# Optimization experiments

Measured on AMD Instinct MI355X. Metric: run time of the kernel, lower is better.

Reference implementation:

```python
import jax, jax.numpy as jnp
import numpy as np

GRID = 3
K = GRID ** 3          # keypoints per proposal (grid rep)
RADIUS = 0.2
NSAMPLE = 16


def _rotz(t):
    c, s = jnp.cos(t), jnp.sin(t)
    z, o = jnp.zeros_like(t), jnp.ones_like(t)
    return jnp.stack([jnp.stack([c, -s, z], -1),
                      jnp.stack([s,  c, z], -1),
                      jnp.stack([z,  z, o], -1)], -2)  # [..., 3, 3]


def _grid_keypoints(boxes, origins, heading):
    # boxes: [B,P,6] = (left,back,down,right,front,up) absolute distances from origin
    B, P, _ = boxes.shape
    ii = jnp.stack(jnp.meshgrid(jnp.arange(GRID), jnp.arange(GRID), jnp.arange(GRID), indexing='ij'), -1)
    dense = ii.reshape(K, 3).astype(boxes.dtype)  # same order as ones(g,g,g).nonzero()
    size = boxes[..., 0:3] + boxes[..., 3:6]                       # [B,P,3]
    local = (dense + 0.5) / GRID * size[:, :, None, :] - boxes[..., None, 0:3]  # [B,P,K,3]
    R = _rotz(heading)                                             # [B,P,3,3]
    pts = jnp.einsum('bpkc,bpcd->bpkd', local, R) + origins[:, :, None, :]
    return pts.reshape(B, P * K, 3)


def _ball_query(key_pts, seed_xyz):
    # key_pts [B,M,3], seed_xyz [B,N,3] -> neighbor indices [B,M,NSAMPLE]
    N = seed_xyz.shape[1]
    d2 = (jnp.sum(key_pts ** 2, -1)[:, :, None]
          + jnp.sum(seed_xyz ** 2, -1)[:, None, :]
          - 2.0 * jnp.einsum('bmc,bnc->bmn', key_pts, seed_xyz))   # [B,M,N]
    cand = jnp.where(d2 < RADIUS ** 2, jnp.arange(N, dtype=jnp.int32), N)
    idx = -jax.lax.top_k(-cand, NSAMPLE)[0]  # first NSAMPLE in-radius indices, ascending
    first = idx[..., 0:1]
    fill = jnp.where(first == N, 0, first)   # empty ball -> index 0 (CUDA kernel default)
    return jnp.where(idx == N, fill, idx)


def _forward(seed_xyz, seed_features, boxes, origins, heading, W1, b1, W2, b2, W3, b3, Wr, br):
    B, P = boxes.shape[:2]
    key_pts = _grid_keypoints(boxes, origins, heading)             # [B,M,3], M=P*K
    idx = _ball_query(key_pts, seed_xyz)                           # [B,M,S]
    b_idx = jnp.arange(B)[:, None, None]
    gx = seed_xyz[b_idx, idx]                                      # [B,M,S,3]
    gf = jnp.transpose(seed_features, (0, 2, 1))[b_idx, idx]       # [B,M,S,C]
    gxyz = (gx - key_pts[:, :, None, :]) / RADIUS                  # normalize_xyz=True
    x = jnp.concatenate([gxyz, gf], -1)                            # use_xyz: [B,M,S,3+C]
    x = jax.nn.relu(x @ W1 + b1)                                   # shared per-point MLP
    x = jax.nn.relu(x @ W2 + b2)
    x = jax.nn.relu(x @ W3 + b3)
    x = jnp.max(x, axis=2)                                         # max-pool over ball -> [B,M,32]
    f = x.reshape(B, P, K, 32)
    # original: [B,32,M] -> view(B,32,P,K) -> transpose(2,3) -> reshape(B,32*K,P)
    f = jnp.transpose(f, (0, 1, 3, 2)).reshape(B, P, 32 * K)       # channel-major (c*K+k) layout
    out = f @ Wr.T + br                                            # 1x1 conv reduce -> [B,P,128]
    return jnp.transpose(out, (0, 2, 1))                           # [B,128,P]


def setup_inputs() -> dict:
    key = jax.random.key(0)
    ks = jax.random.split(key, 9)
    B, N, C, P = 2, 1024, 256, 256
    return {
        'seed_xyz': jax.random.normal(ks[0], (B, N, 3), jnp.float32),
        'seed_features': jax.random.normal(ks[1], (B, C, N), jnp.float32),
        'boxes': jax.random.uniform(ks[2], (B, P, 6), jnp.float32, 0.1, 1.0),
        'origins': jax.random.normal(ks[3], (B, P, 3), jnp.float32),
        'heading': jax.random.uniform(ks[4], (B, P), jnp.float32, 0.0, 6.2831853),
        'W1': jax.random.normal(ks[5], (C + 3, 128), jnp.float32) * 0.05,
        'b1': jnp.zeros((128,), jnp.float32),
        'W2': jax.random.normal(ks[6], (128, 64), jnp.float32) * 0.05,
        'b2': jnp.zeros((64,), jnp.float32),
        'W3': jax.random.normal(ks[7], (64, 32), jnp.float32) * 0.05,
        'b3': jnp.zeros((32,), jnp.float32),
        'Wr': jax.random.normal(ks[8], (128, 32 * K), jnp.float32) * 0.05,
        'br': jnp.zeros((128,), jnp.float32),
    }


def reference(seed_xyz, seed_features, boxes, origins, heading, W1, b1, W2, b2, W3, b3, Wr, br):
    return _forward(seed_xyz, seed_features, boxes, origins, heading, W1, b1, W2, b2, W3, b3, Wr, br)
```

## Files before the change

### kernel.cpp

```cpp
#include <hip/hip_runtime.h>

#define B_ 2
#define N_ 1024
#define C_ 256
#define P_ 256
#define K_ 27
#define M_ (P_ * K_)
#define TOTKP (B_ * M_)
#define NS 16
#define R2C 0.04f
#define QDIM 864


__global__ __launch_bounds__(128) void fpre_k(
    const float* __restrict__ sf, const float* __restrict__ W1,
    const float* __restrict__ b1, float* __restrict__ F)
{
    __shared__ __align__(16) float ssf[C_ * 8];
    int tid = threadIdx.x;
    int bid = blockIdx.x;
    int b = bid >> 7;
    int n0 = (bid & 127) * 8;
    for (int e = tid; e < C_ * 8; e += 128) {
        int c = e >> 3, i = e & 7;
        ssf[e] = sf[(b * C_ + c) * N_ + n0 + i];
    }
    __syncthreads();
    int j = tid;
    float acc[8];
    float bj = b1[j];
#pragma unroll
    for (int i = 0; i < 8; i++) acc[i] = bj;
#pragma unroll 4
    for (int c = 0; c < C_; ++c) {
        float w = W1[(3 + c) * 128 + j];
        const float4* sp = (const float4*)&ssf[c * 8];
        float4 sA = sp[0], sB = sp[1];
        acc[0] = fmaf(sA.x, w, acc[0]); acc[1] = fmaf(sA.y, w, acc[1]);
        acc[2] = fmaf(sA.z, w, acc[2]); acc[3] = fmaf(sA.w, w, acc[3]);
        acc[4] = fmaf(sB.x, w, acc[4]); acc[5] = fmaf(sB.y, w, acc[5]);
        acc[6] = fmaf(sB.z, w, acc[6]); acc[7] = fmaf(sB.w, w, acc[7]);
    }
#pragma unroll
    for (int i = 0; i < 8; i++) F[(b * N_ + n0 + i) * 128 + j] = acc[i];
}

__global__ __launch_bounds__(256) void ballq_k(
    const float* __restrict__ seed_xyz, const float* __restrict__ boxes,
    const float* __restrict__ origins, const float* __restrict__ heading,
    float4* __restrict__ kp4, int* __restrict__ cntw, int* __restrict__ idxw)
{
    int tid = threadIdx.x;
    int wid = tid >> 6, lane = tid & 63;
    int kpg = blockIdx.x * 4 + wid;
    int b = kpg / M_;
    int m = kpg - b * M_;
    int p = m / K_, a = m - p * K_;

    const float* bx = boxes + (b * P_ + p) * 6;
    const float* og = origins + (b * P_ + p) * 3;
    float th = heading[b * P_ + p];
    float di = (float)(a / 9), dj = (float)((a / 3) % 3), dk = (float)(a % 3);
    float s0 = __fadd_rn(bx[0], bx[3]);
    float s1 = __fadd_rn(bx[1], bx[4]);
    float s2 = __fadd_rn(bx[2], bx[5]);
    float lx = __fsub_rn(__fmul_rn(__fdiv_rn(__fadd_rn(di, 0.5f), 3.0f), s0), bx[0]);
    float ly = __fsub_rn(__fmul_rn(__fdiv_rn(__fadd_rn(dj, 0.5f), 3.0f), s1), bx[1]);
    float lz = __fsub_rn(__fmul_rn(__fdiv_rn(__fadd_rn(dk, 0.5f), 3.0f), s2), bx[2]);
    float ct = cosf(th), st = sinf(th);
    float kx = __fadd_rn(__fadd_rn(__fmul_rn(lx, ct), __fmul_rn(ly, st)), og[0]);
    float ky = __fadd_rn(__fadd_rn(__fmul_rn(lx, -st), __fmul_rn(ly, ct)), og[1]);
    float kz = __fadd_rn(lz, og[2]);
    if (lane == 0) kp4[kpg] = make_float4(kx, ky, kz, 0.f);
    float kk = __fadd_rn(__fadd_rn(__fmul_rn(kx, kx), __fmul_rn(ky, ky)), __fmul_rn(kz, kz));

    const float* sb = seed_xyz + b * (N_ * 3) + lane * 48;
    float f[48];
#pragma unroll
    for (int q = 0; q < 12; q++)
        ((float4*)f)[q] = ((const float4*)sb)[q];

    unsigned mask = 0;
#pragma unroll
    for (int i = 0; i < 16; i++) {
        float x = f[3 * i], y = f[3 * i + 1], z = f[3 * i + 2];
        float ss = __fadd_rn(__fadd_rn(__fmul_rn(x, x), __fmul_rn(y, y)), __fmul_rn(z, z));
        float dot = __fadd_rn(__fadd_rn(__fmul_rn(kx, x), __fmul_rn(ky, y)),
                              __fmul_rn(kz, z));
        float d2 = __fsub_rn(__fadd_rn(kk, ss), __fmul_rn(2.0f, dot));
        mask |= (d2 < R2C ? 1u : 0u) << i;
    }

    int pc = __popc(mask);
    int incl = pc;
#pragma unroll
    for (int d = 1; d < 64; d <<= 1) {
        int v = __shfl_up(incl, d);
        if (lane >= d) incl += v;
    }
    int total = __shfl(incl, 63);
    int base = incl - pc;

    int* ip = idxw + kpg * NS;
    unsigned mm = mask;
    while (mm && base < NS) {
        int i = __ffs(mm) - 1;
        mm &= mm - 1;
        ip[base++] = lane * 16 + i;
    }
    if (lane == 0) cntw[kpg] = total < NS ? total : NS;
}

struct Ctx {
    const float* seed; const float* F;
    const float* sW2; const float* sW3;
    float* sH1; float* sH2;
    const int* ip;
    float4 kp;
    float w1x0, w1y0, w1z0, w1x1, w1y1, w1z1, b2j, b3t;
    int lane, t, jh, b, cnt, n0;
};

template <int GS>
static __device__ __forceinline__ void do_group(const Ctx& c, int s0, float& pool)
{
    float gx[GS], gy[GS], gz[GS];
    int nn[GS];
#pragma unroll
    for (int u = 0; u < GS; u++) {
        int s = s0 + u;
        int n = (s < c.cnt) ? c.ip[s] : c.n0;
        nn[u] = n;
        const float* sp = c.seed + (c.b * N_ + n) * 3;
        gx[u] = __fdiv_rn(__fsub_rn(sp[0], c.kp.x), 0.2f);
        gy[u] = __fdiv_rn(__fsub_rn(sp[1], c.kp.y), 0.2f);
        gz[u] = __fdiv_rn(__fsub_rn(sp[2], c.kp.z), 0.2f);
    }
#pragma unroll
    for (int u = 0; u < GS; u++) {
        const float* fp = c.F + (c.b * N_ + nn[u]) * 128;
        float v0 = fp[c.lane];
        float v1 = fp[c.lane + 64];
        v0 = fmaf(gx[u], c.w1x0, fmaf(gy[u], c.w1y0, fmaf(gz[u], c.w1z0, v0)));
        v1 = fmaf(gx[u], c.w1x1, fmaf(gy[u], c.w1y1, fmaf(gz[u], c.w1z1, v1)));
        c.sH1[u * 128 + c.lane] = fmaxf(v0, 0.f);
        c.sH1[u * 128 + c.lane + 64] = fmaxf(v1, 0.f);
    }
    float acc[GS];
#pragma unroll
    for (int u = 0; u < GS; u++) acc[u] = c.b2j;
#pragma unroll
    for (int cc = 0; cc < 128; cc += 4) {
        float w0 = c.sW2[(cc + 0) * 64 + c.lane];
        float w1 = c.sW2[(cc + 1) * 64 + c.lane];
        float w2 = c.sW2[(cc + 2) * 64 + c.lane];
        float w3 = c.sW2[(cc + 3) * 64 + c.lane];
#pragma unroll
        for (int u = 0; u < GS; u++) {
            float4 h = *(const float4*)&c.sH1[u * 128 + cc];
            acc[u] = fmaf(h.x, w0, fmaf(h.y, w1, fmaf(h.z, w2, fmaf(h.w, w3, acc[u]))));
        }
    }
#pragma unroll
    for (int u = 0; u < GS; u++) c.sH2[u * 64 + c.lane] = fmaxf(acc[u], 0.f);
    float a3[GS];
#pragma unroll
    for (int u = 0; u < GS; u++) a3[u] = (c.jh == 0) ? c.b3t : 0.f;
#pragma unroll
    for (int jj = 0; jj < 32; jj += 4) {
        int j0 = c.jh * 32 + jj;
        float w0 = c.sW3[(j0 + 0) * 32 + c.t];
        float w1 = c.sW3[(j0 + 1) * 32 + c.t];
        float w2 = c.sW3[(j0 + 2) * 32 + c.t];
        float w3 = c.sW3[(j0 + 3) * 32 + c.t];
#pragma unroll
        for (int u = 0; u < GS; u++) {
            float4 h = *(const float4*)&c.sH2[u * 64 + j0];
            a3[u] = fmaf(h.x, w0, fmaf(h.y, w1, fmaf(h.z, w2, fmaf(h.w, w3, a3[u]))));
        }
    }
#pragma unroll
    for (int u = 0; u < GS; u++) {
        float v = a3[u] + __shfl_xor(a3[u], 32);
        pool = fmaxf(pool, fmaxf(v, 0.f));
    }
}

__global__ __launch_bounds__(256) void pool_k(
    const float* __restrict__ seed_xyz, const float* __restrict__ F,
    const float* __restrict__ W1, const float* __restrict__ b2g,
    const float* __restrict__ b3g, const float* __restrict__ W2g,
    const float* __restrict__ W3g, const float4* __restrict__ kp4,
    const int* __restrict__ cntw, const int* __restrict__ idxw,
    float* __restrict__ pooled)
{
    __shared__ __align__(16) float sW2[128 * 64];
    __shared__ __align__(16) float sW3[64 * 32];
    __shared__ __align__(16) float sH1[4 * 4 * 128];
    __shared__ __align__(16) float sH2[4 * 4 * 64];
    int tid = threadIdx.x;
    for (int e = tid; e < 2048; e += 256)
        ((float4*)sW2)[e] = ((const float4*)W2g)[e];
    for (int e = tid; e < 512; e += 256)
        ((float4*)sW3)[e] = ((const float4*)W3g)[e];
    __syncthreads();

    int wid = tid >> 6, lane = tid & 63;
    Ctx c;
    c.seed = seed_xyz; c.F = F;
    c.sW2 = sW2; c.sW3 = sW3;
    c.sH1 = sH1 + wid * 4 * 128;
    c.sH2 = sH2 + wid * 4 * 64;
    c.lane = lane; c.t = lane & 31; c.jh = lane >> 5;
    c.w1x0 = W1[lane];       c.w1x1 = W1[lane + 64];
    c.w1y0 = W1[128 + lane]; c.w1y1 = W1[128 + lane + 64];
    c.w1z0 = W1[256 + lane]; c.w1z1 = W1[256 + lane + 64];
    c.b2j = b2g[lane]; c.b3t = b3g[lane & 31];

    for (int i = 0; i < 4; ++i) {
        int kpg = blockIdx.x * 16 + wid * 4 + i;
        c.kp = kp4[kpg];
        c.cnt = cntw[kpg];
        c.ip = idxw + kpg * NS;
        c.b = kpg / M_;
        c.n0 = (c.cnt > 0) ? c.ip[0] : 0;
        int scnt = c.cnt < 1 ? 1 : c.cnt;
        float pool = 0.f;
        for (int s0 = 0; s0 < scnt; s0 += 4) {
            int gs = scnt - s0; gs = gs > 4 ? 4 : gs;
            switch (gs) {
                case 1: do_group<1>(c, s0, pool); break;
                case 2: do_group<2>(c, s0, pool); break;
                case 3: do_group<3>(c, s0, pool); break;
                default: do_group<4>(c, s0, pool); break;
            }
        }
        if (lane < 32) pooled[kpg * 32 + lane] = pool;
    }
}

__global__ __launch_bounds__(256) void wrt_k(const float* __restrict__ Wr,
                                             float* __restrict__ WrT)
{
    int e = blockIdx.x * 256 + threadIdx.x;
    if (e < 128 * QDIM) {
        int j = e / QDIM, q = e - j * QDIM;
        WrT[q * 128 + j] = Wr[e];
    }
}

__global__ __launch_bounds__(256) void final_k(
    const float* __restrict__ pooled, const float* __restrict__ WrT,
    float* __restrict__ partial)
{
    __shared__ __align__(16) float ft[8][108];
    int tid = threadIdx.x;
    int blk = blockIdx.x;
    int c = blk & 7;
    int mt = blk >> 3;
    if (tid < 216) {
        int ri = tid / 27, k = tid - ri * 27;
        int row = mt * 8 + ri;
        int b = row >> 8, p = row & 255;
        const float* sp = pooled + ((b * M_ + p * K_) + k) * 32 + c * 4;
        float4 v = *(const float4*)sp;
        float* fp = &ft[ri][0];
        fp[k] = v.x; fp[27 + k] = v.y; fp[54 + k] = v.z; fp[81 + k] = v.w;
    }
    __syncthreads();
    int j = tid & 127;
    int rh = tid >> 7;
    float a0 = 0.f, a1 = 0.f, a2 = 0.f, a3 = 0.f;
    const float* wp = WrT + (c * 108) * 128 + j;
    const float* f0 = &ft[rh * 4 + 0][0];
    const float* f1 = &ft[rh * 4 + 1][0];
    const float* f2 = &ft[rh * 4 + 2][0];
    const float* f3 = &ft[rh * 4 + 3][0];
#pragma unroll 4
    for (int q = 0; q < 108; ++q) {
        float w = wp[q * 128];
        a0 = fmaf(f0[q], w, a0);
        a1 = fmaf(f1[q], w, a1);
        a2 = fmaf(f2[q], w, a2);
        a3 = fmaf(f3[q], w, a3);
    }
    int row0 = mt * 8 + rh * 4;
    partial[(c * 512 + row0 + 0) * 128 + j] = a0;
    partial[(c * 512 + row0 + 1) * 128 + j] = a1;
    partial[(c * 512 + row0 + 2) * 128 + j] = a2;
    partial[(c * 512 + row0 + 3) * 128 + j] = a3;
}

__global__ __launch_bounds__(256) void fred_k(
    const float* __restrict__ partial, const float* __restrict__ br,
    float* __restrict__ out)
{
    int id = blockIdx.x * 256 + threadIdx.x;
    int j = id & 127;
    int row = id >> 7;
    int b = row >> 8, p = row & 255;
    float s = br[j];
#pragma unroll
    for (int c = 0; c < 8; ++c)
        s += partial[(c * 512 + row) * 128 + j];
    out[(b * 128 + j) * 256 + p] = s;
}

extern "C" void kernel_launch(void* const* d_in, const int* in_sizes, int n_in,
                              void* d_out, int out_size, void* d_ws, size_t ws_size,
                              hipStream_t stream)
{
    const float* seed_xyz  = (const float*)d_in[0];
    const float* seed_feat = (const float*)d_in[1];
    const float* boxes     = (const float*)d_in[2];
    const float* origins   = (const float*)d_in[3];
    const float* heading   = (const float*)d_in[4];
    const float* W1        = (const float*)d_in[5];
    const float* b1        = (const float*)d_in[6];
    const float* W2        = (const float*)d_in[7];
    const float* b2        = (const float*)d_in[8];
    const float* W3        = (const float*)d_in[9];
    const float* b3        = (const float*)d_in[10];
    const float* Wr        = (const float*)d_in[11];
    const float* br        = (const float*)d_in[12];
    float* out = (float*)d_out;

    char* ws = (char*)d_ws;
    float4* kp4    = (float4*)(ws);
    int*    cntw   = (int*)(ws + 221184);
    int*    idxw   = (int*)(ws + 276480);
    float*  F      = (float*)(ws + 1161216);
    float*  pooled = (float*)(ws + 2209792);
    float*  WrT    = (float*)(ws + 3979264);
    float*  part   = (float*)(ws + 4421632);

    fpre_k<<<dim3(256), dim3(128), 0, stream>>>(seed_feat, W1, b1, F);
    ballq_k<<<dim3(3456), dim3(256), 0, stream>>>(seed_xyz, boxes, origins, heading,
                                                  kp4, cntw, idxw);
    wrt_k<<<dim3(432), dim3(256), 0, stream>>>(Wr, WrT);
    pool_k<<<dim3(864), dim3(256), 0, stream>>>(seed_xyz, F, W1, b2, b3, W2, W3,
                                                kp4, cntw, idxw, pooled);
    final_k<<<dim3(512), dim3(256), 0, stream>>>(pooled, WrT, part);
    fred_k<<<dim3(256), dim3(256), 0, stream>>>(part, br, out);
}
```

Measured before the change: 167.4 us.

## Merge prep kernels into one launch, atomic final reduce, smaller pool blocks

Merges the feature precompute, Wr transpose, output bias init and ball query into a single multi-role prep kernel selected by block index. The transpose now reads float4 rows. The final matmul adds its partial sums straight into the output with atomics instead of writing a partial buffer and running a separate reduction kernel. The pooling kernel handles 2 keypoints per wave instead of 4, doubling its grid. This cuts launches and the partial buffer round-trip, but atomic accumulation makes the summation order nondeterministic and adds atomic traffic.

```diff
diff --git a/kernel.cpp b/kernel.cpp
--- a/kernel.cpp
+++ b/kernel.cpp
@@ -12,103 +12,125 @@
 #define QDIM 864
 
 
-__global__ __launch_bounds__(128) void fpre_k(
+#define PREP_FPRE0   0
+#define PREP_WRT0    256
+#define PREP_OINIT0  364
+#define PREP_BALLQ0  620
+#define PREP_NBLK    4076
+
+__global__ __launch_bounds__(256) void prep_k(
     const float* __restrict__ sf, const float* __restrict__ W1,
-    const float* __restrict__ b1, float* __restrict__ F)
+    const float* __restrict__ b1, const float* __restrict__ Wr,
+    const float* __restrict__ br, const float* __restrict__ seed_xyz,
+    const float* __restrict__ boxes, const float* __restrict__ origins,
+    const float* __restrict__ heading,
+    float* __restrict__ F, float* __restrict__ WrT, float* __restrict__ out,
+    float4* __restrict__ kp4, int* __restrict__ cntw, int* __restrict__ idxw)
 {
     __shared__ __align__(16) float ssf[C_ * 8];
     int tid = threadIdx.x;
     int bid = blockIdx.x;
-    int b = bid >> 7;
-    int n0 = (bid & 127) * 8;
-    for (int e = tid; e < C_ * 8; e += 128) {
-        int c = e >> 3, i = e & 7;
-        ssf[e] = sf[(b * C_ + c) * N_ + n0 + i];
-    }
-    __syncthreads();
-    int j = tid;
-    float acc[8];
-    float bj = b1[j];
-#pragma unroll
-    for (int i = 0; i < 8; i++) acc[i] = bj;
-#pragma unroll 4
-    for (int c = 0; c < C_; ++c) {
-        float w = W1[(3 + c) * 128 + j];
-        const float4* sp = (const float4*)&ssf[c * 8];
-        float4 sA = sp[0], sB = sp[1];
-        acc[0] = fmaf(sA.x, w, acc[0]); acc[1] = fmaf(sA.y, w, acc[1]);
-        acc[2] = fmaf(sA.z, w, acc[2]); acc[3] = fmaf(sA.w, w, acc[3]);
-        acc[4] = fmaf(sB.x, w, acc[4]); acc[5] = fmaf(sB.y, w, acc[5]);
-        acc[6] = fmaf(sB.z, w, acc[6]); acc[7] = fmaf(sB.w, w, acc[7]);
-    }
-#pragma unroll
-    for (int i = 0; i < 8; i++) F[(b * N_ + n0 + i) * 128 + j] = acc[i];
-}
-
-__global__ __launch_bounds__(256) void ballq_k(
-    const float* __restrict__ seed_xyz, const float* __restrict__ boxes,
-    const float* __restrict__ origins, const float* __restrict__ heading,
-    float4* __restrict__ kp4, int* __restrict__ cntw, int* __restrict__ idxw)
-{
-    int tid = threadIdx.x;
-    int wid = tid >> 6, lane = tid & 63;
-    int kpg = blockIdx.x * 4 + wid;
-    int b = kpg / M_;
-    int m = kpg - b * M_;
-    int p = m / K_, a = m - p * K_;
-
-    const float* bx = boxes + (b * P_ + p) * 6;
-    const float* og = origins + (b * P_ + p) * 3;
-    float th = heading[b * P_ + p];
-    float di = (float)(a / 9), dj = (float)((a / 3) % 3), dk = (float)(a % 3);
-    float s0 = __fadd_rn(bx[0], bx[3]);
-    float s1 = __fadd_rn(bx[1], bx[4]);
-    float s2 = __fadd_rn(bx[2], bx[5]);
-    float lx = __fsub_rn(__fmul_rn(__fdiv_rn(__fadd_rn(di, 0.5f), 3.0f), s0), bx[0]);
-    float ly = __fsub_rn(__fmul_rn(__fdiv_rn(__fadd_rn(dj, 0.5f), 3.0f), s1), bx[1]);
-    float lz = __fsub_rn(__fmul_rn(__fdiv_rn(__fadd_rn(dk, 0.5f), 3.0f), s2), bx[2]);
-    float ct = cosf(th), st = sinf(th);
-    float kx = __fadd_rn(__fadd_rn(__fmul_rn(lx, ct), __fmul_rn(ly, st)), og[0]);
-    float ky = __fadd_rn(__fadd_rn(__fmul_rn(lx, -st), __fmul_rn(ly, ct)), og[1]);
-    float kz = __fadd_rn(lz, og[2]);
-    if (lane == 0) kp4[kpg] = make_float4(kx, ky, kz, 0.f);
-    float kk = __fadd_rn(__fadd_rn(__fmul_rn(kx, kx), __fmul_rn(ky, ky)), __fmul_rn(kz, kz));
-
-    const float* sb = seed_xyz + b * (N_ * 3) + lane * 48;
-    float f[48];
-#pragma unroll
-    for (int q = 0; q < 12; q++)
-        ((float4*)f)[q] = ((const float4*)sb)[q];
-
-    unsigned mask = 0;
-#pragma unroll
-    for (int i = 0; i < 16; i++) {
-        float x = f[3 * i], y = f[3 * i + 1], z = f[3 * i + 2];
-        float ss = __fadd_rn(__fadd_rn(__fmul_rn(x, x), __fmul_rn(y, y)), __fmul_rn(z, z));
-        float dot = __fadd_rn(__fadd_rn(__fmul_rn(kx, x), __fmul_rn(ky, y)),
-                              __fmul_rn(kz, z));
-        float d2 = __fsub_rn(__fadd_rn(kk, ss), __fmul_rn(2.0f, dot));
-        mask |= (d2 < R2C ? 1u : 0u) << i;
-    }
-
-    int pc = __popc(mask);
-    int incl = pc;
-#pragma unroll
-    for (int d = 1; d < 64; d <<= 1) {
-        int v = __shfl_up(incl, d);
-        if (lane >= d) incl += v;
-    }
-    int total = __shfl(incl, 63);
-    int base = incl - pc;
-
-    int* ip = idxw + kpg * NS;
-    unsigned mm = mask;
-    while (mm && base < NS) {
-        int i = __ffs(mm) - 1;
-        mm &= mm - 1;
-        ip[base++] = lane * 16 + i;
-    }
-    if (lane == 0) cntw[kpg] = total < NS ? total : NS;
+
+    if (bid < PREP_WRT0) {
+        int b = bid >> 7;
+        int n0 = (bid & 127) * 8;
+        for (int e = tid; e < C_ * 8; e += 256) {
+            int c = e >> 3, i = e & 7;
+            ssf[e] = sf[(b * C_ + c) * N_ + n0 + i];
+        }
+        __syncthreads();
+        int j = tid & 127;
+        int h = tid >> 7;
+        float acc[4];
+        float bj = b1[j];
+#pragma unroll
+        for (int i = 0; i < 4; i++) acc[i] = bj;
+#pragma unroll 8
+        for (int c = 0; c < C_; ++c) {
+            float w = W1[(3 + c) * 128 + j];
+            float4 s = *(const float4*)&ssf[c * 8 + h * 4];
+            acc[0] = fmaf(s.x, w, acc[0]);
+            acc[1] = fmaf(s.y, w, acc[1]);
+            acc[2] = fmaf(s.z, w, acc[2]);
+            acc[3] = fmaf(s.w, w, acc[3]);
+        }
+#pragma unroll
+        for (int i = 0; i < 4; i++)
+            F[(b * N_ + n0 + h * 4 + i) * 128 + j] = acc[i];
+    } else if (bid < PREP_OINIT0) {
+        int e4 = (bid - PREP_WRT0) * 256 + tid;
+        int j = e4 / 216, qq = e4 - j * 216;
+        float4 v = ((const float4*)(Wr + j * QDIM))[qq];
+        int q0 = qq * 4;
+        WrT[(q0 + 0) * 128 + j] = v.x;
+        WrT[(q0 + 1) * 128 + j] = v.y;
+        WrT[(q0 + 2) * 128 + j] = v.z;
+        WrT[(q0 + 3) * 128 + j] = v.w;
+    } else if (bid < PREP_BALLQ0) {
+        int id = (bid - PREP_OINIT0) * 256 + tid;
+        out[id] = br[(id >> 8) & 127];
+    } else {
+        int wid = tid >> 6, lane = tid & 63;
+        int kpg = (bid - PREP_BALLQ0) * 4 + wid;
+        int b = kpg / M_;
+        int m = kpg - b * M_;
+        int p = m / K_, a = m - p * K_;
+
+        const float* bx = boxes + (b * P_ + p) * 6;
+        const float* og = origins + (b * P_ + p) * 3;
+        float th = heading[b * P_ + p];
+        float di = (float)(a / 9), dj = (float)((a / 3) % 3), dk = (float)(a % 3);
+        float s0 = __fadd_rn(bx[0], bx[3]);
+        float s1 = __fadd_rn(bx[1], bx[4]);
+        float s2 = __fadd_rn(bx[2], bx[5]);
+        float lx = __fsub_rn(__fmul_rn(__fdiv_rn(__fadd_rn(di, 0.5f), 3.0f), s0), bx[0]);
+        float ly = __fsub_rn(__fmul_rn(__fdiv_rn(__fadd_rn(dj, 0.5f), 3.0f), s1), bx[1]);
+        float lz = __fsub_rn(__fmul_rn(__fdiv_rn(__fadd_rn(dk, 0.5f), 3.0f), s2), bx[2]);
+        float ct = cosf(th), st = sinf(th);
+        float kx = __fadd_rn(__fadd_rn(__fmul_rn(lx, ct), __fmul_rn(ly, st)), og[0]);
+        float ky = __fadd_rn(__fadd_rn(__fmul_rn(lx, -st), __fmul_rn(ly, ct)), og[1]);
+        float kz = __fadd_rn(lz, og[2]);
+        if (lane == 0) kp4[kpg] = make_float4(kx, ky, kz, 0.f);
+        float kk = __fadd_rn(__fadd_rn(__fmul_rn(kx, kx), __fmul_rn(ky, ky)),
+                             __fmul_rn(kz, kz));
+
+        const float* sb = seed_xyz + b * (N_ * 3) + lane * 48;
+        float f[48];
+#pragma unroll
+        for (int q = 0; q < 12; q++)
+            ((float4*)f)[q] = ((const float4*)sb)[q];
+
+        unsigned mask = 0;
+#pragma unroll
+        for (int i = 0; i < 16; i++) {
+            float x = f[3 * i], y = f[3 * i + 1], z = f[3 * i + 2];
+            float ss = __fadd_rn(__fadd_rn(__fmul_rn(x, x), __fmul_rn(y, y)),
+                                 __fmul_rn(z, z));
+            float dot = __fadd_rn(__fadd_rn(__fmul_rn(kx, x), __fmul_rn(ky, y)),
+                                  __fmul_rn(kz, z));
+            float d2 = __fsub_rn(__fadd_rn(kk, ss), __fmul_rn(2.0f, dot));
+            mask |= (d2 < R2C ? 1u : 0u) << i;
+        }
+
+        int pc = __popc(mask);
+        int incl = pc;
+#pragma unroll
+        for (int d = 1; d < 64; d <<= 1) {
+            int v = __shfl_up(incl, d);
+            if (lane >= d) incl += v;
+        }
+        int total = __shfl(incl, 63);
+        int base = incl - pc;
+
+        int* ip = idxw + kpg * NS;
+        unsigned mm = mask;
+        while (mm && base < NS) {
+            int i = __ffs(mm) - 1;
+            mm &= mm - 1;
+            ip[base++] = lane * 16 + i;
+        }
+        if (lane == 0) cntw[kpg] = total < NS ? total : NS;
+    }
 }
 
 struct Ctx {
@@ -217,8 +239,8 @@
     c.w1z0 = W1[256 + lane]; c.w1z1 = W1[256 + lane + 64];
     c.b2j = b2g[lane]; c.b3t = b3g[lane & 31];
 
-    for (int i = 0; i < 4; ++i) {
-        int kpg = blockIdx.x * 16 + wid * 4 + i;
+    for (int i = 0; i < 2; ++i) {
+        int kpg = blockIdx.x * 8 + wid * 2 + i;
         c.kp = kp4[kpg];
         c.cnt = cntw[kpg];
         c.ip = idxw + kpg * NS;
@@ -239,19 +261,9 @@
     }
 }
 
-__global__ __launch_bounds__(256) void wrt_k(const float* __restrict__ Wr,
-                                             float* __restrict__ WrT)
-{
-    int e = blockIdx.x * 256 + threadIdx.x;
-    if (e < 128 * QDIM) {
-        int j = e / QDIM, q = e - j * QDIM;
-        WrT[q * 128 + j] = Wr[e];
-    }
-}
-
 __global__ __launch_bounds__(256) void final_k(
     const float* __restrict__ pooled, const float* __restrict__ WrT,
-    float* __restrict__ partial)
+    float* __restrict__ out)
 {
     __shared__ __align__(16) float ft[8][108];
     int tid = threadIdx.x;
@@ -285,25 +297,13 @@
         a3 = fmaf(f3[q], w, a3);
     }
     int row0 = mt * 8 + rh * 4;
-    partial[(c * 512 + row0 + 0) * 128 + j] = a0;
-    partial[(c * 512 + row0 + 1) * 128 + j] = a1;
-    partial[(c * 512 + row0 + 2) * 128 + j] = a2;
-    partial[(c * 512 + row0 + 3) * 128 + j] = a3;
-}
-
-__global__ __launch_bounds__(256) void fred_k(
-    const float* __restrict__ partial, const float* __restrict__ br,
-    float* __restrict__ out)
-{
-    int id = blockIdx.x * 256 + threadIdx.x;
-    int j = id & 127;
-    int row = id >> 7;
-    int b = row >> 8, p = row & 255;
-    float s = br[j];
-#pragma unroll
-    for (int c = 0; c < 8; ++c)
-        s += partial[(c * 512 + row) * 128 + j];
-    out[(b * 128 + j) * 256 + p] = s;
+    int b0 = row0 >> 8;
+    int p0 = row0 & 255;
+    float* op = out + b0 * 128 * 256 + j * 256 + p0;
+    atomicAdd(op + 0, a0);
+    atomicAdd(op + 1, a1);
+    atomicAdd(op + 2, a2);
+    atomicAdd(op + 3, a3);
 }
 
 extern "C" void kernel_launch(void* const* d_in, const int* in_sizes, int n_in,
@@ -332,14 +332,11 @@
     float*  F      = (float*)(ws + 1161216);
     float*  pooled = (float*)(ws + 2209792);
     float*  WrT    = (float*)(ws + 3979264);
-    float*  part   = (float*)(ws + 4421632);
-
-    fpre_k<<<dim3(256), dim3(128), 0, stream>>>(seed_feat, W1, b1, F);
-    ballq_k<<<dim3(3456), dim3(256), 0, stream>>>(seed_xyz, boxes, origins, heading,
-                                                  kp4, cntw, idxw);
-    wrt_k<<<dim3(432), dim3(256), 0, stream>>>(Wr, WrT);
-    pool_k<<<dim3(864), dim3(256), 0, stream>>>(seed_xyz, F, W1, b2, b3, W2, W3,
-                                                kp4, cntw, idxw, pooled);
-    final_k<<<dim3(512), dim3(256), 0, stream>>>(pooled, WrT, part);
-    fred_k<<<dim3(256), dim3(256), 0, stream>>>(part, br, out);
-}
+
+    prep_k<<<dim3(PREP_NBLK), dim3(256), 0, stream>>>(
+        seed_feat, W1, b1, Wr, br, seed_xyz, boxes, origins, heading,
+        F, WrT, out, kp4, cntw, idxw);
+    pool_k<<<dim3(1728), dim3(256), 0, stream>>>(seed_xyz, F, W1, b2, b3, W2, W3,
+                                                 kp4, cntw, idxw, pooled);
+    final_k<<<dim3(512), dim3(256), 0, stream>>>(pooled, WrT, out);
+}
```

After: 162.0 us. 3.2% less time.
